# Kernel optimization log

Measured on AMD Instinct MI355X. Metric: run time of the kernel, lower is better.

Reference implementation:

```python
import jax, jax.numpy as jnp
import numpy as np

N_NODES = 100000
N_EDGES = 3200000
NUM_GRAPHS = 64
NEG_SLOPE = 0.2  # PyG GATConv default leaky_relu slope


def gat_conv(x, src, dst, W, att_src, att_dst, bias, heads, out_ch, concat):
    """PyG GATConv (default args: add_self_loops=True, negative_slope=0.2).
    src/dst already include self loops."""
    n = x.shape[0]
    h = (x @ W).reshape(n, heads, out_ch)              # [N,H,C]
    a_src = jnp.sum(h * att_src, axis=-1)              # [N,H]
    a_dst = jnp.sum(h * att_dst, axis=-1)              # [N,H]
    e = jax.nn.leaky_relu(a_src[src] + a_dst[dst], NEG_SLOPE)  # [E,H]
    # segment softmax over destination nodes
    m = jax.ops.segment_max(e, dst, num_segments=n)
    ex = jnp.exp(e - m[dst])
    denom = jax.ops.segment_sum(ex, dst, num_segments=n)
    alpha = ex / (denom[dst] + 1e-16)                  # [E,H]
    msg = h[src] * alpha[:, :, None]                   # [E,H,C]
    out = jax.ops.segment_sum(msg, dst, num_segments=n)  # [N,H,C]
    if concat:
        out = out.reshape(n, heads * out_ch)
    else:
        out = out.mean(axis=1)
    return out + bias


def setup_inputs() -> dict:
    key = jax.random.key(0)
    ks = jax.random.split(key, 12)
    x = jax.random.normal(ks[0], (N_NODES, 4), dtype=jnp.float32)
    edge_index = jax.random.randint(ks[1], (2, N_EDGES), 0, N_NODES, dtype=jnp.int64)
    batch = jnp.sort(jax.random.randint(ks[2], (N_NODES,), 0, NUM_GRAPHS, dtype=jnp.int64))
    s = 0.1
    return {
        "x": x,
        "edge_index": edge_index,
        "batch": batch,
        "W1": jax.random.normal(ks[3], (4, 64), dtype=jnp.float32) * s,
        "att_src1": jax.random.normal(ks[4], (2, 32), dtype=jnp.float32) * s,
        "att_dst1": jax.random.normal(ks[5], (2, 32), dtype=jnp.float32) * s,
        "bias1": jnp.zeros((64,), dtype=jnp.float32),
        "W2": jax.random.normal(ks[6], (64, 64), dtype=jnp.float32) * s,
        "att_src2": jax.random.normal(ks[7], (1, 64), dtype=jnp.float32) * s,
        "att_dst2": jax.random.normal(ks[8], (1, 64), dtype=jnp.float32) * s,
        "bias2": jnp.zeros((64,), dtype=jnp.float32),
    }


def reference(x, edge_index, batch, W1, att_src1, att_dst1, bias1, W2, att_src2, att_dst2, bias2):
    n = x.shape[0]
    loops = jnp.arange(n, dtype=edge_index.dtype)
    src = jnp.concatenate([edge_index[0], loops])
    dst = jnp.concatenate([edge_index[1], loops])
    h = gat_conv(x, src, dst, W1, att_src1, att_dst1, bias1, heads=2, out_ch=32, concat=True)
    h = jax.nn.elu(h)
    # dropout is identity in eval mode
    h = gat_conv(h, src, dst, W2, att_src2, att_dst2, bias2, heads=1, out_ch=64, concat=False)
    # global_mean_pool
    sums = jax.ops.segment_sum(h, batch, num_segments=NUM_GRAPHS)
    counts = jax.ops.segment_sum(jnp.ones((n,), h.dtype), batch, num_segments=NUM_GRAPHS)
    return sums / jnp.maximum(counts, 1.0)[:, None]
```

## Files before the change

### kernel.cpp

```cpp
#include <hip/hip_runtime.h>
#include <hip/hip_bf16.h>
#include <hip/hip_fp16.h>
#include <math.h>


__device__ __forceinline__ float leaky(float x) { return x >= 0.f ? x : 0.2f * x; }
__device__ __forceinline__ int iclamp(int v, int lo, int hi) {
  return v < lo ? lo : (v > hi ? hi : v);
}
__device__ __forceinline__ unsigned char f8(float v) {
  return (unsigned char)(__builtin_amdgcn_cvt_pk_fp8_f32(v, v, 0, false) & 0xff);
}

typedef __attribute__((ext_vector_type(8))) _Float16 f16x8;
typedef __attribute__((ext_vector_type(4))) float f32x4;
typedef __attribute__((ext_vector_type(2))) float f32x2;

#define NBUCK 1024
#define BSHIFT 7
#define BCAP 4608
#define CSRSZ (NBUCK * BCAP)
#define MAXR 8

__global__ __launch_bounds__(256) void k_att1(
    const float* __restrict__ x, const float* __restrict__ W1,
    const float* __restrict__ att_src1, const float* __restrict__ att_dst1,
    float* __restrict__ a_src1, float* __restrict__ a_dst1, int n) {
  __shared__ float W1s[256];
  int t = threadIdx.x;
  W1s[t] = W1[t];
  __syncthreads();
  int node = blockIdx.x * 4 + (t >> 6);
  int lane = t & 63;
  if (node >= n) return;
  float4 xr = ((const float4*)x)[node];
  float h = xr.x * W1s[lane] + xr.y * W1s[64 + lane] + xr.z * W1s[128 + lane] + xr.w * W1s[192 + lane];
  float vs = h * att_src1[lane];
  float vd = h * att_dst1[lane];
  #pragma unroll
  for (int m = 16; m >= 1; m >>= 1) { vs += __shfl_xor(vs, m); vd += __shfl_xor(vd, m); }
  if ((lane & 31) == 0) {
    int head = lane >> 5;
    a_src1[node * 2 + head] = vs;
    a_dst1[node * 2 + head] = vd;
  }
}

__global__ __launch_bounds__(1024, 8) void k_bscatter(
    const int* __restrict__ ei, int E, int n, int* __restrict__ bcur,
    unsigned* __restrict__ pairs) {
  __shared__ int h[NBUCK];
  __shared__ int cur[NBUCK];
  int t = threadIdx.x;
  if (t < NBUCK) h[t] = 0;
  __syncthreads();
  int chunk = (E + gridDim.x - 1) / gridDim.x;
  int beg = blockIdx.x * chunk;
  int end = beg + chunk; if (end > E) end = E;
  unsigned pR[MAXR];
  unsigned short bR[MAXR];
  int cntr = 0;
  for (int i = beg + t; i < end && cntr < MAXR; i += 1024) {
    int s = iclamp(ei[i], 0, n - 1);
    int d = iclamp(ei[E + i], 0, n - 1);
    int bkt = d >> BSHIFT;
    pR[cntr] = ((unsigned)(d & 127) << 25) | (unsigned)s;
    bR[cntr] = (unsigned short)bkt;
    atomicAdd(&h[bkt], 1);
    ++cntr;
  }
  __syncthreads();
  if (t < NBUCK) cur[t] = t * BCAP + (h[t] ? atomicAdd(&bcur[t], h[t]) : 0);
  __syncthreads();
  for (int k = 0; k < cntr; ++k) {
    int bkt = bR[k];
    int pos = atomicAdd(&cur[bkt], 1);
    if (pos >= bkt * BCAP && pos < (bkt + 1) * BCAP) pairs[pos] = pR[k];
  }
}

__global__ __launch_bounds__(256) void k_bbuild(
    const unsigned* __restrict__ pairs, const int* __restrict__ bcur,
    int n, int* __restrict__ rowbeg, int* __restrict__ rowend,
    int* __restrict__ csr) {
  int b = blockIdx.x;
  int node0 = b << BSHIFT;
  if (node0 >= n) return;
  int base = b * BCAP;
  int cnt = iclamp(bcur[b], 0, BCAP);
  __shared__ int sh[128];
  __shared__ int cur[128];
  int t = threadIdx.x;
  if (t < 128) sh[t] = 0;
  __syncthreads();
  for (int i = t; i < cnt; i += 256)
    atomicAdd(&sh[pairs[base + i] >> 25], 1);
  __syncthreads();
  int v = (t < 128) ? sh[t] : 0;
  for (int ofs = 1; ofs < 128; ofs <<= 1) {
    int u = (t >= ofs && t < 128) ? sh[t - ofs] : 0;
    __syncthreads();
    if (t < 128) sh[t] += u;
    __syncthreads();
  }
  if (t < 128) {
    int off = sh[t] - v;
    cur[t] = off;
    int node = node0 + t;
    if (node < n) {
      rowbeg[node] = base + off;
      rowend[node] = base + off + v;
    }
  }
  __syncthreads();
  for (int i = t; i < cnt; i += 256) {
    unsigned p = pairs[base + i];
    int l = p >> 25;
    int r = atomicAdd(&cur[l], 1);
    int pos = base + r;
    if (pos >= 0 && pos < CSRSZ) csr[pos] = (int)(p & 0x1ffffffu);
  }
}

__global__ __launch_bounds__(256) void k_gat1(
    const float* __restrict__ x, const float* __restrict__ W1,
    const float* __restrict__ a_src1, const float* __restrict__ a_dst1,
    const int* __restrict__ rowbeg, const int* __restrict__ rowend,
    const int* __restrict__ csr,
    const float* __restrict__ bias1, __half* __restrict__ hB,
    int n) {
  __shared__ float W1s[256];
  int t = threadIdx.x;
  W1s[t] = W1[t];
  __syncthreads();
  int lane = t & 63;
  int nd = lane >> 4, sub = lane & 15;
  int node = (blockIdx.x * 4 + (t >> 6)) * 4 + nd;
  bool valid = node < n;
  int nc = valid ? node : 0;
  int beg = valid ? iclamp(rowbeg[nc], 0, CSRSZ) : 0;
  int end = valid ? iclamp(rowend[nc], beg, CSRSZ) : 0;
  float2 ad = ((const float2*)a_dst1)[nc];
  const float4* xp = (const float4*)x;
  const float2* asp = (const float2*)a_src1;
  float A0 = 0.f, A1 = 0.f, A2 = 0.f, A3 = 0.f, dn0 = 0.f;
  float B0 = 0.f, B1 = 0.f, B2 = 0.f, B3 = 0.f, dn1 = 0.f;
  int e = beg + sub;
  for (; e + 16 < end; e += 32) {
    int sa = iclamp(csr[e], 0, n - 1);
    int sb = iclamp(csr[e + 16], 0, n - 1);
    float2 asa = asp[sa];
    float2 asb = asp[sb];
    float4 xa = xp[sa];
    float4 xb = xp[sb];
    float ea0 = __expf(leaky(asa.x + ad.x));
    float ea1 = __expf(leaky(asa.y + ad.y));
    float eb0 = __expf(leaky(asb.x + ad.x));
    float eb1 = __expf(leaky(asb.y + ad.y));
    dn0 += ea0 + eb0; dn1 += ea1 + eb1;
    A0 = fmaf(ea0, xa.x, A0); A1 = fmaf(ea0, xa.y, A1);
    A2 = fmaf(ea0, xa.z, A2); A3 = fmaf(ea0, xa.w, A3);
    B0 = fmaf(ea1, xa.x, B0); B1 = fmaf(ea1, xa.y, B1);
    B2 = fmaf(ea1, xa.z, B2); B3 = fmaf(ea1, xa.w, B3);
    A0 = fmaf(eb0, xb.x, A0); A1 = fmaf(eb0, xb.y, A1);
    A2 = fmaf(eb0, xb.z, A2); A3 = fmaf(eb0, xb.w, A3);
    B0 = fmaf(eb1, xb.x, B0); B1 = fmaf(eb1, xb.y, B1);
    B2 = fmaf(eb1, xb.z, B2); B3 = fmaf(eb1, xb.w, B3);
  }
  if (e < end) {
    int s = iclamp(csr[e], 0, n - 1);
    float2 as = asp[s];
    float ex0 = __expf(leaky(as.x + ad.x));
    float ex1 = __expf(leaky(as.y + ad.y));
    float4 xr = xp[s];
    dn0 += ex0; dn1 += ex1;
    A0 = fmaf(ex0, xr.x, A0); A1 = fmaf(ex0, xr.y, A1);
    A2 = fmaf(ex0, xr.z, A2); A3 = fmaf(ex0, xr.w, A3);
    B0 = fmaf(ex1, xr.x, B0); B1 = fmaf(ex1, xr.y, B1);
    B2 = fmaf(ex1, xr.z, B2); B3 = fmaf(ex1, xr.w, B3);
  }
  bool lo = (sub < 8);
  float C0, C1, C2, C3, dnC, sA, sB;
  sA = __shfl_xor(A0, 8); sB = __shfl_xor(B0, 8); C0 = lo ? A0 + sA : B0 + sB;
  sA = __shfl_xor(A1, 8); sB = __shfl_xor(B1, 8); C1 = lo ? A1 + sA : B1 + sB;
  sA = __shfl_xor(A2, 8); sB = __shfl_xor(B2, 8); C2 = lo ? A2 + sA : B2 + sB;
  sA = __shfl_xor(A3, 8); sB = __shfl_xor(B3, 8); C3 = lo ? A3 + sA : B3 + sB;
  sA = __shfl_xor(dn0, 8); sB = __shfl_xor(dn1, 8); dnC = lo ? dn0 + sA : dn1 + sB;
  #pragma unroll
  for (int m = 4; m >= 1; m >>= 1) {
    C0 += __shfl_xor(C0, m); C1 += __shfl_xor(C1, m);
    C2 += __shfl_xor(C2, m); C3 += __shfl_xor(C3, m);
    dnC += __shfl_xor(dnC, m);
  }
  float2 asn = asp[nc];
  float4 xs = xp[nc];
  float exs = __expf(leaky((lo ? asn.x : asn.y) + (lo ? ad.x : ad.y)));
  dnC += exs;
  C0 = fmaf(exs, xs.x, C0); C1 = fmaf(exs, xs.y, C1);
  C2 = fmaf(exs, xs.z, C2); C3 = fmaf(exs, xs.w, C3);
  float inv = 1.0f / (dnC + 1e-16f);
  if (valid) {
    int f0 = sub * 4;
    float vv[4];
    #pragma unroll
    for (int i = 0; i < 4; ++i) {
      int f = f0 + i;
      float accv = C0 * W1s[f] + C1 * W1s[64 + f] + C2 * W1s[128 + f] + C3 * W1s[192 + f];
      float v = accv * inv + bias1[f];
      vv[i] = v > 0.f ? v : expm1f(v);
    }
    __half2 h01 = __float22half2_rn(make_float2(vv[0], vv[1]));
    __half2 h23 = __float22half2_rn(make_float2(vv[2], vv[3]));
    uint2 pk;
    pk.x = *(unsigned*)&h01;
    pk.y = *(unsigned*)&h23;
    *(uint2*)(hB + (size_t)node * 64 + f0) = pk;
  }
}

__global__ __launch_bounds__(256) void k_lin2(
    const __half* __restrict__ hB, const float* __restrict__ W2,
    const float* __restrict__ att_src2, const float* __restrict__ att_dst2,
    float* __restrict__ a_src2, float* __restrict__ a_dst2,
    unsigned char* __restrict__ hC, int n) {
  __shared__ __attribute__((aligned(16))) _Float16 Whi[64 * 72];
  __shared__ __attribute__((aligned(16))) _Float16 Wlo[64 * 72];
  int t = threadIdx.x;
  for (int i = t; i < 4096; i += 256) {
    int k = i >> 6, col = i & 63;
    float w = W2[i];
    _Float16 hi = (_Float16)w;
    _Float16 lo = (_Float16)(w - (float)hi);
    Whi[col * 72 + k] = hi;
    Wlo[col * 72 + k] = lo;
  }
  __syncthreads();
  int wave = t >> 6, lane = t & 63;
  int quad = lane >> 4, c = lane & 15;
  float as2[4], ad2[4];
  #pragma unroll
  for (int tt = 0; tt < 4; ++tt) {
    as2[tt] = att_src2[tt * 16 + c];
    ad2[tt] = att_dst2[tt * 16 + c];
  }
  for (int it = 0; it < 4; ++it) {
    int m0 = blockIdx.x * 256 + wave * 64 + it * 16;
    if (m0 >= n) break;
    int mrow = m0 + c; if (mrow > n - 1) mrow = n - 1;
    const _Float16* hrow = (const _Float16*)(hB + (size_t)mrow * 64);
    f16x8 a0 = *(const f16x8*)(hrow + quad * 8);
    f16x8 a1 = *(const f16x8*)(hrow + 32 + quad * 8);
    f32x4 zero = {0.f, 0.f, 0.f, 0.f};
    f32x4 acc[4] = {zero, zero, zero, zero};
    #pragma unroll
    for (int tt = 0; tt < 4; ++tt) {
      int nn = tt * 16 + c;
      const _Float16* wh = &Whi[nn * 72];
      const _Float16* wl = &Wlo[nn * 72];
      f16x8 bh0 = *(const f16x8*)(wh + quad * 8);
      f16x8 bh1 = *(const f16x8*)(wh + 32 + quad * 8);
      f16x8 bl0 = *(const f16x8*)(wl + quad * 8);
      f16x8 bl1 = *(const f16x8*)(wl + 32 + quad * 8);
      acc[tt] = __builtin_amdgcn_mfma_f32_16x16x32_f16(a0, bh0, acc[tt], 0, 0, 0);
      acc[tt] = __builtin_amdgcn_mfma_f32_16x16x32_f16(a1, bh1, acc[tt], 0, 0, 0);
      acc[tt] = __builtin_amdgcn_mfma_f32_16x16x32_f16(a0, bl0, acc[tt], 0, 0, 0);
      acc[tt] = __builtin_amdgcn_mfma_f32_16x16x32_f16(a1, bl1, acc[tt], 0, 0, 0);
    }
    #pragma unroll
    for (int r = 0; r < 4; ++r) {
      float s = 0.f, d = 0.f;
      #pragma unroll
      for (int tt = 0; tt < 4; ++tt) {
        s = fmaf(acc[tt][r], as2[tt], s);
        d = fmaf(acc[tt][r], ad2[tt], d);
      }
      #pragma unroll
      for (int msk = 8; msk >= 1; msk >>= 1) {
        s += __shfl_xor(s, msk);
        d += __shfl_xor(d, msk);
      }
      int m = m0 + quad * 4 + r;
      if (m < n) {
        if (c == 0) { a_src2[m] = s; a_dst2[m] = d; }
        unsigned char* orow = hC + (size_t)m * 64;
        #pragma unroll
        for (int tt = 0; tt < 4; ++tt)
          orow[tt * 16 + c] = f8(acc[tt][r]);
      }
    }
  }
}

__global__ __launch_bounds__(256) void k_gat2(
    const unsigned char* __restrict__ hC, const float* __restrict__ a_src2,
    const float* __restrict__ a_dst2, const int* __restrict__ rowbeg,
    const int* __restrict__ rowend, const int* __restrict__ csr,
    const float* __restrict__ bias2,
    __half* __restrict__ h2, int n) {
  __shared__ unsigned long long stage[4 * 64];
  int t = threadIdx.x;
  int w = t >> 6, lane = t & 63;
  int node = blockIdx.x * 4 + w;
  if (node >= n) return;
  int beg = iclamp(rowbeg[node], 0, CSRSZ);
  int end = iclamp(rowend[node], beg, CSRSZ);
  float ad = a_dst2[node];
  int g = lane >> 3;
  int p = lane & 7;
  const uint2* hrows = (const uint2*)hC;
  unsigned long long* st = &stage[w * 64];
  float ac0 = 0.f, ac1 = 0.f, ac2 = 0.f, ac3 = 0.f;
  float ac4 = 0.f, ac5 = 0.f, ac6 = 0.f, ac7 = 0.f;
  float dn = 0.f;
  for (int tb = beg; tb < end; tb += 64) {
    int tc = end - tb; if (tc > 64) tc = 64;
    int s = 0; float ex = 0.f;
    if (lane < tc) {
      s = iclamp(csr[tb + lane], 0, n - 1);
      ex = __expf(leaky(a_src2[s] + ad));
    }
    dn += ex;
    st[lane] = ((unsigned long long)(unsigned)s << 32) | (unsigned)__float_as_uint(ex);
    int steps = (tc + 7) >> 3;
    int j = 0;
    for (; j + 2 <= steps; j += 2) {
      unsigned long long pk0 = st[j * 8 + g];
      unsigned long long pk1 = st[(j + 1) * 8 + g];
      int s0 = (int)(pk0 >> 32), s1 = (int)(pk1 >> 32);
      float e0 = __uint_as_float((unsigned)pk0);
      float e1 = __uint_as_float((unsigned)pk1);
      uint2 hw0 = hrows[(size_t)s0 * 8 + p];
      uint2 hw1 = hrows[(size_t)s1 * 8 + p];
      f32x2 a, b;
      a = __builtin_amdgcn_cvt_pk_f32_fp8(hw0.x, false);
      b = __builtin_amdgcn_cvt_pk_f32_fp8(hw0.x, true);
      ac0 = fmaf(e0, a.x, ac0); ac1 = fmaf(e0, a.y, ac1);
      ac2 = fmaf(e0, b.x, ac2); ac3 = fmaf(e0, b.y, ac3);
      a = __builtin_amdgcn_cvt_pk_f32_fp8(hw0.y, false);
      b = __builtin_amdgcn_cvt_pk_f32_fp8(hw0.y, true);
      ac4 = fmaf(e0, a.x, ac4); ac5 = fmaf(e0, a.y, ac5);
      ac6 = fmaf(e0, b.x, ac6); ac7 = fmaf(e0, b.y, ac7);
      a = __builtin_amdgcn_cvt_pk_f32_fp8(hw1.x, false);
      b = __builtin_amdgcn_cvt_pk_f32_fp8(hw1.x, true);
      ac0 = fmaf(e1, a.x, ac0); ac1 = fmaf(e1, a.y, ac1);
      ac2 = fmaf(e1, b.x, ac2); ac3 = fmaf(e1, b.y, ac3);
      a = __builtin_amdgcn_cvt_pk_f32_fp8(hw1.y, false);
      b = __builtin_amdgcn_cvt_pk_f32_fp8(hw1.y, true);
      ac4 = fmaf(e1, a.x, ac4); ac5 = fmaf(e1, a.y, ac5);
      ac6 = fmaf(e1, b.x, ac6); ac7 = fmaf(e1, b.y, ac7);
    }
    if (j < steps) {
      unsigned long long pk0 = st[j * 8 + g];
      int s0 = (int)(pk0 >> 32);
      float e0 = __uint_as_float((unsigned)pk0);
      uint2 hw0 = hrows[(size_t)s0 * 8 + p];
      f32x2 a, b;
      a = __builtin_amdgcn_cvt_pk_f32_fp8(hw0.x, false);
      b = __builtin_amdgcn_cvt_pk_f32_fp8(hw0.x, true);
      ac0 = fmaf(e0, a.x, ac0); ac1 = fmaf(e0, a.y, ac1);
      ac2 = fmaf(e0, b.x, ac2); ac3 = fmaf(e0, b.y, ac3);
      a = __builtin_amdgcn_cvt_pk_f32_fp8(hw0.y, false);
      b = __builtin_amdgcn_cvt_pk_f32_fp8(hw0.y, true);
      ac4 = fmaf(e0, a.x, ac4); ac5 = fmaf(e0, a.y, ac5);
      ac6 = fmaf(e0, b.x, ac6); ac7 = fmaf(e0, b.y, ac7);
    }
  }
  #pragma unroll
  for (int m = 8; m <= 32; m <<= 1) {
    ac0 += __shfl_xor(ac0, m); ac1 += __shfl_xor(ac1, m);
    ac2 += __shfl_xor(ac2, m); ac3 += __shfl_xor(ac3, m);
    ac4 += __shfl_xor(ac4, m); ac5 += __shfl_xor(ac5, m);
    ac6 += __shfl_xor(ac6, m); ac7 += __shfl_xor(ac7, m);
  }
  #pragma unroll
  for (int m = 32; m >= 1; m >>= 1) dn += __shfl_xor(dn, m);
  float exs = __expf(leaky(a_src2[node] + ad));
  dn += exs;
  uint2 hs = hrows[(size_t)node * 8 + p];
  {
    f32x2 a, b;
    a = __builtin_amdgcn_cvt_pk_f32_fp8(hs.x, false);
    b = __builtin_amdgcn_cvt_pk_f32_fp8(hs.x, true);
    ac0 = fmaf(exs, a.x, ac0); ac1 = fmaf(exs, a.y, ac1);
    ac2 = fmaf(exs, b.x, ac2); ac3 = fmaf(exs, b.y, ac3);
    a = __builtin_amdgcn_cvt_pk_f32_fp8(hs.y, false);
    b = __builtin_amdgcn_cvt_pk_f32_fp8(hs.y, true);
    ac4 = fmaf(exs, a.x, ac4); ac5 = fmaf(exs, a.y, ac5);
    ac6 = fmaf(exs, b.x, ac6); ac7 = fmaf(exs, b.y, ac7);
  }
  if (g == 0) {
    float inv = 1.0f / (dn + 1e-16f);
    const float* b2 = bias2 + p * 8;
    __half2 o0 = __float22half2_rn(make_float2(ac0 * inv + b2[0], ac1 * inv + b2[1]));
    __half2 o1 = __float22half2_rn(make_float2(ac2 * inv + b2[2], ac3 * inv + b2[3]));
    __half2 o2 = __float22half2_rn(make_float2(ac4 * inv + b2[4], ac5 * inv + b2[5]));
    __half2 o3 = __float22half2_rn(make_float2(ac6 * inv + b2[6], ac7 * inv + b2[7]));
    uint4 pk;
    pk.x = *(unsigned*)&o0; pk.y = *(unsigned*)&o1;
    pk.z = *(unsigned*)&o2; pk.w = *(unsigned*)&o3;
    ((uint4*)(h2 + (size_t)node * 64))[p] = pk;
  }
}

__global__ __launch_bounds__(256) void k_pool(
    const __half* __restrict__ h2, const int* __restrict__ batch,
    float* __restrict__ pool, float* __restrict__ cnt, int n, int G) {
  const int PW = 64;
  int wave = blockIdx.x * 4 + (threadIdx.x >> 6);
  int lane = threadIdx.x & 63;
  int start = wave * PW;
  if (start >= n) return;
  int end = start + PW; if (end > n) end = n;
  int bcur = iclamp(batch[start], 0, G - 1);
  float acc = 0.f, count = 0.f;
  for (int i = start; i < end; ++i) {
    int b = iclamp(batch[i], 0, G - 1);
    if (b != bcur) {
      atomicAdd(&pool[bcur * 64 + lane], acc);
      if (lane == 0) atomicAdd(&cnt[bcur], count);
      bcur = b; acc = 0.f; count = 0.f;
    }
    acc += __half2float(h2[(size_t)i * 64 + lane]);
    count += 1.f;
  }
  atomicAdd(&pool[bcur * 64 + lane], acc);
  if (lane == 0) atomicAdd(&cnt[bcur], count);
}

__global__ void k_final(const float* __restrict__ pool, const float* __restrict__ cnt,
                        float* __restrict__ out, int G) {
  int i = blockIdx.x * blockDim.x + threadIdx.x;
  if (i >= G * 64) return;
  out[i] = pool[i] / fmaxf(cnt[i >> 6], 1.0f);
}

extern "C" void kernel_launch(void* const* d_in, const int* in_sizes, int n_in,
                              void* d_out, int out_size, void* d_ws, size_t ws_size,
                              hipStream_t stream) {
  const float* x        = (const float*)d_in[0];
  const int*   ei       = (const int*)d_in[1];
  const int*   batch    = (const int*)d_in[2];
  const float* W1       = (const float*)d_in[3];
  const float* att_src1 = (const float*)d_in[4];
  const float* att_dst1 = (const float*)d_in[5];
  const float* bias1    = (const float*)d_in[6];
  const float* W2       = (const float*)d_in[7];
  const float* att_src2 = (const float*)d_in[8];
  const float* att_dst2 = (const float*)d_in[9];
  const float* bias2    = (const float*)d_in[10];

  const int n = in_sizes[0] / 4;
  const int E = in_sizes[1] / 2;
  const int G = out_size / 64;

  char* p = (char*)d_ws;
  auto alloc = [&](size_t bytes) -> void* {
    void* r = (void*)p;
    p += (bytes + 255) & ~(size_t)255;
    return r;
  };
  int* csr = (int*)alloc((size_t)CSRSZ * 4);
  size_t hsz = (size_t)n * 64 * 2;
  size_t csz = (size_t)n * 64;
  size_t rsz = hsz + csz;
  if (rsz < (size_t)CSRSZ * 4) rsz = (size_t)CSRSZ * 4;
  char* R = (char*)alloc(rsz);
  unsigned* pairs = (unsigned*)R;
  __half* hB = (__half*)R;
  __half* h2 = (__half*)R;
  unsigned char* hC = (unsigned char*)(R + hsz);
  int*   rowbeg = (int*)alloc((size_t)n * 4);
  int*   rowend = (int*)alloc((size_t)n * 4);
  size_t poolelems = (size_t)G * 64 + G;
  char*  Z = (char*)alloc(poolelems * 4 + (size_t)NBUCK * 4);
  float* pool = (float*)Z;
  float* cnt  = pool + (size_t)G * 64;
  int*   bcur = (int*)(Z + poolelems * 4);
  float* a_src1 = (float*)alloc((size_t)n * 2 * 4);
  float* a_dst1 = (float*)alloc((size_t)n * 2 * 4);
  float* a_src2 = (float*)alloc((size_t)n * 4);
  float* a_dst2 = (float*)alloc((size_t)n * 4);

  hipMemsetAsync(Z, 0, poolelems * 4 + (size_t)NBUCK * 4, stream);

  const int gridN4 = (n + 3) / 4;
  int NBK = (E + MAXR * 1024 - 1) / (MAXR * 1024);
  if (NBK < 512) NBK = 512;

  k_att1<<<gridN4, 256, 0, stream>>>(x, W1, att_src1, att_dst1, a_src1, a_dst1, n);
  k_bscatter<<<NBK, 1024, 0, stream>>>(ei, E, n, bcur, pairs);
  k_bbuild<<<NBUCK, 256, 0, stream>>>(pairs, bcur, n, rowbeg, rowend, csr);
  k_gat1<<<(n + 15) / 16, 256, 0, stream>>>(x, W1, a_src1, a_dst1, rowbeg, rowend, csr, bias1, hB, n);
  k_lin2<<<(n + 255) / 256, 256, 0, stream>>>(hB, W2, att_src2, att_dst2, a_src2, a_dst2, hC, n);
  k_gat2<<<gridN4, 256, 0, stream>>>(hC, a_src2, a_dst2, rowbeg, rowend, csr, bias2, h2, n);
  k_pool<<<(n + 255) / 256, 256, 0, stream>>>(h2, batch, pool, cnt, n, G);
  k_final<<<(G * 64 + 255) / 256, 256, 0, stream>>>(pool, cnt, (float*)d_out, G);
}
```

Measured before the change: 292.4 us.

## Fuse attention-score prep into scatter and CSR build into layer-1 aggregation

Result: faster. 279.8 us (-4.3%).

```diff
diff --git a/kernel.cpp b/kernel.cpp
--- a/kernel.cpp
+++ b/kernel.cpp
@@ -22,39 +22,38 @@
 #define CSRSZ (NBUCK * BCAP)
 #define MAXR 8
 
-__global__ __launch_bounds__(256) void k_att1(
+__global__ __launch_bounds__(1024, 8) void k_scatt(
+    const int* __restrict__ ei, int E, int n, int* __restrict__ bcur,
+    unsigned* __restrict__ pairs,
     const float* __restrict__ x, const float* __restrict__ W1,
     const float* __restrict__ att_src1, const float* __restrict__ att_dst1,
-    float* __restrict__ a_src1, float* __restrict__ a_dst1, int n) {
+    float* __restrict__ a_src1, float* __restrict__ a_dst1, int NBK) {
+  __shared__ int h[NBUCK];
+  __shared__ int cur[NBUCK];
   __shared__ float W1s[256];
   int t = threadIdx.x;
-  W1s[t] = W1[t];
-  __syncthreads();
-  int node = blockIdx.x * 4 + (t >> 6);
-  int lane = t & 63;
-  if (node >= n) return;
-  float4 xr = ((const float4*)x)[node];
-  float h = xr.x * W1s[lane] + xr.y * W1s[64 + lane] + xr.z * W1s[128 + lane] + xr.w * W1s[192 + lane];
-  float vs = h * att_src1[lane];
-  float vd = h * att_dst1[lane];
-  #pragma unroll
-  for (int m = 16; m >= 1; m >>= 1) { vs += __shfl_xor(vs, m); vd += __shfl_xor(vd, m); }
-  if ((lane & 31) == 0) {
-    int head = lane >> 5;
-    a_src1[node * 2 + head] = vs;
-    a_dst1[node * 2 + head] = vd;
-  }
-}
-
-__global__ __launch_bounds__(1024, 8) void k_bscatter(
-    const int* __restrict__ ei, int E, int n, int* __restrict__ bcur,
-    unsigned* __restrict__ pairs) {
-  __shared__ int h[NBUCK];
-  __shared__ int cur[NBUCK];
-  int t = threadIdx.x;
+  if (blockIdx.x >= NBK) {
+    if (t < 256) W1s[t] = W1[t];
+    __syncthreads();
+    int node = (blockIdx.x - NBK) * 16 + (t >> 6);
+    int lane = t & 63;
+    if (node >= n) return;
+    float4 xr = ((const float4*)x)[node];
+    float hv = xr.x * W1s[lane] + xr.y * W1s[64 + lane] + xr.z * W1s[128 + lane] + xr.w * W1s[192 + lane];
+    float vs = hv * att_src1[lane];
+    float vd = hv * att_dst1[lane];
+    #pragma unroll
+    for (int m = 16; m >= 1; m >>= 1) { vs += __shfl_xor(vs, m); vd += __shfl_xor(vd, m); }
+    if ((lane & 31) == 0) {
+      int head = lane >> 5;
+      a_src1[node * 2 + head] = vs;
+      a_dst1[node * 2 + head] = vd;
+    }
+    return;
+  }
   if (t < NBUCK) h[t] = 0;
   __syncthreads();
-  int chunk = (E + gridDim.x - 1) / gridDim.x;
+  int chunk = (E + NBK - 1) / NBK;
   int beg = blockIdx.x * chunk;
   int end = beg + chunk; if (end > E) end = E;
   unsigned pR[MAXR];
@@ -79,18 +78,26 @@
   }
 }
 
-__global__ __launch_bounds__(256) void k_bbuild(
+__global__ __launch_bounds__(256) void k_bgat1(
     const unsigned* __restrict__ pairs, const int* __restrict__ bcur,
-    int n, int* __restrict__ rowbeg, int* __restrict__ rowend,
-    int* __restrict__ csr) {
+    const float* __restrict__ x, const float* __restrict__ W1,
+    const float* __restrict__ a_src1, const float* __restrict__ a_dst1,
+    const float* __restrict__ bias1,
+    int* __restrict__ rowbeg, int* __restrict__ rowend, int* __restrict__ csr,
+    __half* __restrict__ hB, int n) {
+  __shared__ int lcsr[BCAP];
+  __shared__ int sh[128];
+  __shared__ int cur[128];
+  __shared__ int lrb[128];
+  __shared__ int lre[128];
+  __shared__ float W1s[256];
+  int t = threadIdx.x;
+  W1s[t] = W1[t];
   int b = blockIdx.x;
   int node0 = b << BSHIFT;
   if (node0 >= n) return;
   int base = b * BCAP;
   int cnt = iclamp(bcur[b], 0, BCAP);
-  __shared__ int sh[128];
-  __shared__ int cur[128];
-  int t = threadIdx.x;
   if (t < 128) sh[t] = 0;
   __syncthreads();
   for (int i = t; i < cnt; i += 256)
@@ -106,6 +113,8 @@
   if (t < 128) {
     int off = sh[t] - v;
     cur[t] = off;
+    lrb[t] = off;
+    lre[t] = off + v;
     int node = node0 + t;
     if (node < n) {
       rowbeg[node] = base + off;
@@ -117,104 +126,98 @@
     unsigned p = pairs[base + i];
     int l = p >> 25;
     int r = atomicAdd(&cur[l], 1);
-    int pos = base + r;
-    if (pos >= 0 && pos < CSRSZ) csr[pos] = (int)(p & 0x1ffffffu);
-  }
-}
-
-__global__ __launch_bounds__(256) void k_gat1(
-    const float* __restrict__ x, const float* __restrict__ W1,
-    const float* __restrict__ a_src1, const float* __restrict__ a_dst1,
-    const int* __restrict__ rowbeg, const int* __restrict__ rowend,
-    const int* __restrict__ csr,
-    const float* __restrict__ bias1, __half* __restrict__ hB,
-    int n) {
-  __shared__ float W1s[256];
-  int t = threadIdx.x;
-  W1s[t] = W1[t];
-  __syncthreads();
-  int lane = t & 63;
-  int nd = lane >> 4, sub = lane & 15;
-  int node = (blockIdx.x * 4 + (t >> 6)) * 4 + nd;
-  bool valid = node < n;
-  int nc = valid ? node : 0;
-  int beg = valid ? iclamp(rowbeg[nc], 0, CSRSZ) : 0;
-  int end = valid ? iclamp(rowend[nc], beg, CSRSZ) : 0;
-  float2 ad = ((const float2*)a_dst1)[nc];
+    if (r >= 0 && r < BCAP) lcsr[r] = (int)(p & 0x1ffffffu);
+  }
+  __syncthreads();
+  for (int i = t; i < cnt; i += 256)
+    csr[base + i] = lcsr[i];
+  int wave = t >> 6, lane = t & 63;
+  int nd = (lane >> 4), sub = lane & 15;
   const float4* xp = (const float4*)x;
   const float2* asp = (const float2*)a_src1;
-  float A0 = 0.f, A1 = 0.f, A2 = 0.f, A3 = 0.f, dn0 = 0.f;
-  float B0 = 0.f, B1 = 0.f, B2 = 0.f, B3 = 0.f, dn1 = 0.f;
-  int e = beg + sub;
-  for (; e + 16 < end; e += 32) {
-    int sa = iclamp(csr[e], 0, n - 1);
-    int sb = iclamp(csr[e + 16], 0, n - 1);
-    float2 asa = asp[sa];
-    float2 asb = asp[sb];
-    float4 xa = xp[sa];
-    float4 xb = xp[sb];
-    float ea0 = __expf(leaky(asa.x + ad.x));
-    float ea1 = __expf(leaky(asa.y + ad.y));
-    float eb0 = __expf(leaky(asb.x + ad.x));
-    float eb1 = __expf(leaky(asb.y + ad.y));
-    dn0 += ea0 + eb0; dn1 += ea1 + eb1;
-    A0 = fmaf(ea0, xa.x, A0); A1 = fmaf(ea0, xa.y, A1);
-    A2 = fmaf(ea0, xa.z, A2); A3 = fmaf(ea0, xa.w, A3);
-    B0 = fmaf(ea1, xa.x, B0); B1 = fmaf(ea1, xa.y, B1);
-    B2 = fmaf(ea1, xa.z, B2); B3 = fmaf(ea1, xa.w, B3);
-    A0 = fmaf(eb0, xb.x, A0); A1 = fmaf(eb0, xb.y, A1);
-    A2 = fmaf(eb0, xb.z, A2); A3 = fmaf(eb0, xb.w, A3);
-    B0 = fmaf(eb1, xb.x, B0); B1 = fmaf(eb1, xb.y, B1);
-    B2 = fmaf(eb1, xb.z, B2); B3 = fmaf(eb1, xb.w, B3);
-  }
-  if (e < end) {
-    int s = iclamp(csr[e], 0, n - 1);
-    float2 as = asp[s];
-    float ex0 = __expf(leaky(as.x + ad.x));
-    float ex1 = __expf(leaky(as.y + ad.y));
-    float4 xr = xp[s];
-    dn0 += ex0; dn1 += ex1;
-    A0 = fmaf(ex0, xr.x, A0); A1 = fmaf(ex0, xr.y, A1);
-    A2 = fmaf(ex0, xr.z, A2); A3 = fmaf(ex0, xr.w, A3);
-    B0 = fmaf(ex1, xr.x, B0); B1 = fmaf(ex1, xr.y, B1);
-    B2 = fmaf(ex1, xr.z, B2); B3 = fmaf(ex1, xr.w, B3);
-  }
-  bool lo = (sub < 8);
-  float C0, C1, C2, C3, dnC, sA, sB;
-  sA = __shfl_xor(A0, 8); sB = __shfl_xor(B0, 8); C0 = lo ? A0 + sA : B0 + sB;
-  sA = __shfl_xor(A1, 8); sB = __shfl_xor(B1, 8); C1 = lo ? A1 + sA : B1 + sB;
-  sA = __shfl_xor(A2, 8); sB = __shfl_xor(B2, 8); C2 = lo ? A2 + sA : B2 + sB;
-  sA = __shfl_xor(A3, 8); sB = __shfl_xor(B3, 8); C3 = lo ? A3 + sA : B3 + sB;
-  sA = __shfl_xor(dn0, 8); sB = __shfl_xor(dn1, 8); dnC = lo ? dn0 + sA : dn1 + sB;
-  #pragma unroll
-  for (int m = 4; m >= 1; m >>= 1) {
-    C0 += __shfl_xor(C0, m); C1 += __shfl_xor(C1, m);
-    C2 += __shfl_xor(C2, m); C3 += __shfl_xor(C3, m);
-    dnC += __shfl_xor(dnC, m);
-  }
-  float2 asn = asp[nc];
-  float4 xs = xp[nc];
-  float exs = __expf(leaky((lo ? asn.x : asn.y) + (lo ? ad.x : ad.y)));
-  dnC += exs;
-  C0 = fmaf(exs, xs.x, C0); C1 = fmaf(exs, xs.y, C1);
-  C2 = fmaf(exs, xs.z, C2); C3 = fmaf(exs, xs.w, C3);
-  float inv = 1.0f / (dnC + 1e-16f);
-  if (valid) {
-    int f0 = sub * 4;
-    float vv[4];
+  for (int rnd = 0; rnd < 8; ++rnd) {
+    int nodeLocal = rnd * 16 + wave * 4 + nd;
+    int node = node0 + nodeLocal;
+    bool valid = node < n;
+    int nc = valid ? node : 0;
+    int ebeg = valid ? lrb[nodeLocal] : 0;
+    int eend = valid ? lre[nodeLocal] : 0;
+    ebeg = iclamp(ebeg, 0, BCAP);
+    eend = iclamp(eend, ebeg, BCAP);
+    float2 ad = ((const float2*)a_dst1)[nc];
+    float A0 = 0.f, A1 = 0.f, A2 = 0.f, A3 = 0.f, dn0 = 0.f;
+    float B0 = 0.f, B1 = 0.f, B2 = 0.f, B3 = 0.f, dn1 = 0.f;
+    int e = ebeg + sub;
+    for (; e + 16 < eend; e += 32) {
+      int sa = iclamp(lcsr[e], 0, n - 1);
+      int sb = iclamp(lcsr[e + 16], 0, n - 1);
+      float2 asa = asp[sa];
+      float2 asb = asp[sb];
+      float4 xa = xp[sa];
+      float4 xb = xp[sb];
+      float ea0 = __expf(leaky(asa.x + ad.x));
+      float ea1 = __expf(leaky(asa.y + ad.y));
+      float eb0 = __expf(leaky(asb.x + ad.x));
+      float eb1 = __expf(leaky(asb.y + ad.y));
+      dn0 += ea0 + eb0; dn1 += ea1 + eb1;
+      A0 = fmaf(ea0, xa.x, A0); A1 = fmaf(ea0, xa.y, A1);
+      A2 = fmaf(ea0, xa.z, A2); A3 = fmaf(ea0, xa.w, A3);
+      B0 = fmaf(ea1, xa.x, B0); B1 = fmaf(ea1, xa.y, B1);
+      B2 = fmaf(ea1, xa.z, B2); B3 = fmaf(ea1, xa.w, B3);
+      A0 = fmaf(eb0, xb.x, A0); A1 = fmaf(eb0, xb.y, A1);
+      A2 = fmaf(eb0, xb.z, A2); A3 = fmaf(eb0, xb.w, A3);
+      B0 = fmaf(eb1, xb.x, B0); B1 = fmaf(eb1, xb.y, B1);
+      B2 = fmaf(eb1, xb.z, B2); B3 = fmaf(eb1, xb.w, B3);
+    }
+    if (e < eend) {
+      int s = iclamp(lcsr[e], 0, n - 1);
+      float2 as = asp[s];
+      float ex0 = __expf(leaky(as.x + ad.x));
+      float ex1 = __expf(leaky(as.y + ad.y));
+      float4 xr = xp[s];
+      dn0 += ex0; dn1 += ex1;
+      A0 = fmaf(ex0, xr.x, A0); A1 = fmaf(ex0, xr.y, A1);
+      A2 = fmaf(ex0, xr.z, A2); A3 = fmaf(ex0, xr.w, A3);
+      B0 = fmaf(ex1, xr.x, B0); B1 = fmaf(ex1, xr.y, B1);
+      B2 = fmaf(ex1, xr.z, B2); B3 = fmaf(ex1, xr.w, B3);
+    }
+    bool lo = (sub < 8);
+    float C0, C1, C2, C3, dnC, sA, sB;
+    sA = __shfl_xor(A0, 8); sB = __shfl_xor(B0, 8); C0 = lo ? A0 + sA : B0 + sB;
+    sA = __shfl_xor(A1, 8); sB = __shfl_xor(B1, 8); C1 = lo ? A1 + sA : B1 + sB;
+    sA = __shfl_xor(A2, 8); sB = __shfl_xor(B2, 8); C2 = lo ? A2 + sA : B2 + sB;
+    sA = __shfl_xor(A3, 8); sB = __shfl_xor(B3, 8); C3 = lo ? A3 + sA : B3 + sB;
+    sA = __shfl_xor(dn0, 8); sB = __shfl_xor(dn1, 8); dnC = lo ? dn0 + sA : dn1 + sB;
     #pragma unroll
-    for (int i = 0; i < 4; ++i) {
-      int f = f0 + i;
-      float accv = C0 * W1s[f] + C1 * W1s[64 + f] + C2 * W1s[128 + f] + C3 * W1s[192 + f];
-      float v = accv * inv + bias1[f];
-      vv[i] = v > 0.f ? v : expm1f(v);
-    }
-    __half2 h01 = __float22half2_rn(make_float2(vv[0], vv[1]));
-    __half2 h23 = __float22half2_rn(make_float2(vv[2], vv[3]));
-    uint2 pk;
-    pk.x = *(unsigned*)&h01;
-    pk.y = *(unsigned*)&h23;
-    *(uint2*)(hB + (size_t)node * 64 + f0) = pk;
+    for (int m = 4; m >= 1; m >>= 1) {
+      C0 += __shfl_xor(C0, m); C1 += __shfl_xor(C1, m);
+      C2 += __shfl_xor(C2, m); C3 += __shfl_xor(C3, m);
+      dnC += __shfl_xor(dnC, m);
+    }
+    float2 asn = asp[nc];
+    float4 xs = xp[nc];
+    float exs = __expf(leaky((lo ? asn.x : asn.y) + (lo ? ad.x : ad.y)));
+    dnC += exs;
+    C0 = fmaf(exs, xs.x, C0); C1 = fmaf(exs, xs.y, C1);
+    C2 = fmaf(exs, xs.z, C2); C3 = fmaf(exs, xs.w, C3);
+    float inv = 1.0f / (dnC + 1e-16f);
+    if (valid) {
+      int f0 = sub * 4;
+      float vv[4];
+      #pragma unroll
+      for (int i = 0; i < 4; ++i) {
+        int f = f0 + i;
+        float accv = C0 * W1s[f] + C1 * W1s[64 + f] + C2 * W1s[128 + f] + C3 * W1s[192 + f];
+        float vx = accv * inv + bias1[f];
+        vv[i] = vx > 0.f ? vx : expm1f(vx);
+      }
+      __half2 h01 = __float22half2_rn(make_float2(vv[0], vv[1]));
+      __half2 h23 = __float22half2_rn(make_float2(vv[2], vv[3]));
+      uint2 pk;
+      pk.x = *(unsigned*)&h01;
+      pk.y = *(unsigned*)&h23;
+      *(uint2*)(hB + (size_t)node * 64 + f0) = pk;
+    }
   }
 }
 
@@ -409,22 +412,23 @@
   int wave = blockIdx.x * 4 + (threadIdx.x >> 6);
   int lane = threadIdx.x & 63;
   int start = wave * PW;
-  if (start >= n) return;
-  int end = start + PW; if (end > n) end = n;
-  int bcur = iclamp(batch[start], 0, G - 1);
-  float acc = 0.f, count = 0.f;
-  for (int i = start; i < end; ++i) {
-    int b = iclamp(batch[i], 0, G - 1);
-    if (b != bcur) {
-      atomicAdd(&pool[bcur * 64 + lane], acc);
-      if (lane == 0) atomicAdd(&cnt[bcur], count);
-      bcur = b; acc = 0.f; count = 0.f;
-    }
-    acc += __half2float(h2[(size_t)i * 64 + lane]);
-    count += 1.f;
-  }
-  atomicAdd(&pool[bcur * 64 + lane], acc);
-  if (lane == 0) atomicAdd(&cnt[bcur], count);
+  if (start < n) {
+    int end = start + PW; if (end > n) end = n;
+    int bcur = iclamp(batch[start], 0, G - 1);
+    float acc = 0.f, count = 0.f;
+    for (int i = start; i < end; ++i) {
+      int b = iclamp(batch[i], 0, G - 1);
+      if (b != bcur) {
+        atomicAdd(&pool[bcur * 64 + lane], acc);
+        if (lane == 0) atomicAdd(&cnt[bcur], count);
+        bcur = b; acc = 0.f; count = 0.f;
+      }
+      acc += __half2float(h2[(size_t)i * 64 + lane]);
+      count += 1.f;
+    }
+    atomicAdd(&pool[bcur * 64 + lane], acc);
+    if (lane == 0) atomicAdd(&cnt[bcur], count);
+  }
 }
 
 __global__ void k_final(const float* __restrict__ pool, const float* __restrict__ cnt,
@@ -459,13 +463,10 @@
     p += (bytes + 255) & ~(size_t)255;
     return r;
   };
-  int* csr = (int*)alloc((size_t)CSRSZ * 4);
+  unsigned* pairs = (unsigned*)alloc((size_t)CSRSZ * 4);
+  int* csr = (int*)pairs;
   size_t hsz = (size_t)n * 64 * 2;
-  size_t csz = (size_t)n * 64;
-  size_t rsz = hsz + csz;
-  if (rsz < (size_t)CSRSZ * 4) rsz = (size_t)CSRSZ * 4;
-  char* R = (char*)alloc(rsz);
-  unsigned* pairs = (unsigned*)R;
+  char* R = (char*)alloc(hsz + (size_t)n * 64);
   __half* hB = (__half*)R;
   __half* h2 = (__half*)R;
   unsigned char* hC = (unsigned char*)(R + hsz);
@@ -483,16 +484,16 @@
 
   hipMemsetAsync(Z, 0, poolelems * 4 + (size_t)NBUCK * 4, stream);
 
-  const int gridN4 = (n + 3) / 4;
   int NBK = (E + MAXR * 1024 - 1) / (MAXR * 1024);
   if (NBK < 512) NBK = 512;
-
-  k_att1<<<gridN4, 256, 0, stream>>>(x, W1, att_src1, att_dst1, a_src1, a_dst1, n);
-  k_bscatter<<<NBK, 1024, 0, stream>>>(ei, E, n, bcur, pairs);
-  k_bbuild<<<NBUCK, 256, 0, stream>>>(pairs, bcur, n, rowbeg, rowend, csr);
-  k_gat1<<<(n + 15) / 16, 256, 0, stream>>>(x, W1, a_src1, a_dst1, rowbeg, rowend, csr, bias1, hB, n);
+  int natt = (n + 15) / 16;
+
+  k_scatt<<<NBK + natt, 1024, 0, stream>>>(ei, E, n, bcur, pairs,
+                                           x, W1, att_src1, att_dst1, a_src1, a_dst1, NBK);
+  k_bgat1<<<NBUCK, 256, 0, stream>>>(pairs, bcur, x, W1, a_src1, a_dst1, bias1,
+                                     rowbeg, rowend, csr, hB, n);
   k_lin2<<<(n + 255) / 256, 256, 0, stream>>>(hB, W2, att_src2, att_dst2, a_src2, a_dst2, hC, n);
-  k_gat2<<<gridN4, 256, 0, stream>>>(hC, a_src2, a_dst2, rowbeg, rowend, csr, bias2, h2, n);
+  k_gat2<<<(n + 3) / 4, 256, 0, stream>>>(hC, a_src2, a_dst2, rowbeg, rowend, csr, bias2, h2, n);
   k_pool<<<(n + 255) / 256, 256, 0, stream>>>(h2, batch, pool, cnt, n, G);
   k_final<<<(G * 64 + 255) / 256, 256, 0, stream>>>(pool, cnt, (float*)d_out, G);
 }
```
